# Kernel optimization log

Measured on AMD Instinct MI355X. Metric: run time of the kernel, lower is better.

## Reference

```python
import jax, jax.numpy as jnp
import numpy as np

N = 50000
E = 800000
F_IN = 512
HID = 32
HEADS = 8
CLS = 64
NEG_SLOPE = 0.2
EPS = 1e-16  # PyG softmax denominator epsilon


def setup_inputs() -> dict:
    key = jax.random.key(0)
    ks = jax.random.split(key, 10)
    x = jax.random.normal(ks[0], (N, F_IN), dtype=jnp.float32)
    edge_index = jax.random.randint(ks[1], (2, E), 0, N, dtype=jnp.int64)
    # layer 1: in=F_IN, heads=HEADS, out_per_head=HID, concat
    s1 = 1.0 / np.sqrt(F_IN)
    W1 = jax.random.normal(ks[2], (F_IN, HEADS * HID), dtype=jnp.float32) * s1
    att_src1 = jax.random.normal(ks[3], (HEADS, HID), dtype=jnp.float32) * 0.1
    att_dst1 = jax.random.normal(ks[4], (HEADS, HID), dtype=jnp.float32) * 0.1
    b1 = jnp.zeros((HEADS * HID,), dtype=jnp.float32)
    # layer 2: in=HEADS*HID, heads=1, out=CLS, no concat
    s2 = 1.0 / np.sqrt(HEADS * HID)
    W2 = jax.random.normal(ks[5], (HEADS * HID, CLS), dtype=jnp.float32) * s2
    att_src2 = jax.random.normal(ks[6], (1, CLS), dtype=jnp.float32) * 0.1
    att_dst2 = jax.random.normal(ks[7], (1, CLS), dtype=jnp.float32) * 0.1
    b2 = jnp.zeros((CLS,), dtype=jnp.float32)
    return {"x": x, "edge_index": edge_index,
            "W1": W1, "att_src1": att_src1, "att_dst1": att_dst1, "b1": b1,
            "W2": W2, "att_src2": att_src2, "att_dst2": att_dst2, "b2": b2}


def gat_conv(x, edge_index, W, att_src, att_dst, bias, concat):
    n = x.shape[0]
    heads, c = att_src.shape
    h = (x @ W).reshape(n, heads, c)                       # [N,H,C]
    # add self loops (PyG GATConv default)
    loop = jnp.arange(n, dtype=edge_index.dtype)
    src = jnp.concatenate([edge_index[0], loop])
    dst = jnp.concatenate([edge_index[1], loop])
    a_src = jnp.einsum('nhc,hc->nh', h, att_src)           # [N,H]
    a_dst = jnp.einsum('nhc,hc->nh', h, att_dst)
    e = a_src[src] + a_dst[dst]                            # [E',H]
    e = jax.nn.leaky_relu(e, NEG_SLOPE)
    # segment softmax over destination node
    m = jax.ops.segment_max(e, dst, num_segments=n)
    e = jnp.exp(e - jax.lax.stop_gradient(m)[dst])
    s = jax.ops.segment_sum(e, dst, num_segments=n)
    alpha = e / (s[dst] + EPS)                             # [E',H]
    msg = h[src] * alpha[:, :, None]                       # [E',H,C]
    out = jax.ops.segment_sum(msg, dst, num_segments=n)    # [N,H,C]
    out = out.reshape(n, heads * c) if concat else out.mean(axis=1)
    return out + bias


def reference(x, edge_index, W1, att_src1, att_dst1, b1, W2, att_src2, att_dst2, b2):
    h = gat_conv(x, edge_index, W1, att_src1, att_dst1, b1, concat=True)
    h = jax.nn.relu(h)
    # F.dropout with training=False (eval) is identity
    h = gat_conv(h, edge_index, W2, att_src2, att_dst2, b2, concat=False)
    return jax.nn.log_softmax(h, axis=1)
```

## Files before the change

kernel.cpp:

```cpp
#include <hip/hip_runtime.h>
#include <hip/hip_bf16.h>
#include <stdint.h>

#define F_IN 512
#define HID 32
#define HEADS 8
#define C1 (HEADS*HID)
#define CLS 64
#define NEG 0.2f
#define EPS 1e-16f

typedef __bf16 bf16x8 __attribute__((ext_vector_type(8)));
typedef __bf16 bf16x4 __attribute__((ext_vector_type(4)));
typedef float  f32x4  __attribute__((ext_vector_type(4)));

__device__ __forceinline__ float leaky(float v) { return v > 0.f ? v : NEG * v; }

__device__ __forceinline__ bf16x8 cvt8(float4 a, float4 b) {
  bf16x8 o;
  o[0] = (__bf16)a.x; o[1] = (__bf16)a.y; o[2] = (__bf16)a.z; o[3] = (__bf16)a.w;
  o[4] = (__bf16)b.x; o[5] = (__bf16)b.y; o[6] = (__bf16)b.z; o[7] = (__bf16)b.w;
  return o;
}

__global__ __launch_bounds__(256) void prep(const float* __restrict__ W1,
    const float* __restrict__ W2, const int* __restrict__ ei,
    __bf16* __restrict__ w1t, __bf16* __restrict__ w2t,
    int* __restrict__ deg, int E) {
  const int b = blockIdx.x, t = threadIdx.x;
  if (b < 64) {
    int i = b * 256 + t;
    int o0 = i * 8;
    int c = o0 >> 9, k0 = o0 & 511;
    bf16x8 o;
#pragma unroll
    for (int j = 0; j < 8; j++) o[j] = (__bf16)W1[(size_t)(k0 + j) * C1 + c];
    *(bf16x8*)(w1t + (size_t)o0) = o;
  } else if (b < 72) {
    int i = (b - 64) * 256 + t;
    int o0 = i * 8;
    int c = o0 >> 8, k0 = o0 & 255;
    bf16x8 o;
#pragma unroll
    for (int j = 0; j < 8; j++) o[j] = (__bf16)W2[(size_t)(k0 + j) * CLS + c];
    *(bf16x8*)(w2t + (size_t)o0) = o;
  } else {
    int e = (b - 72) * 256 + t;
    if (e < E) atomicAdd(&deg[ei[E + e]], 1);
  }
}

__global__ __launch_bounds__(256) void scan_k1(const int* __restrict__ deg,
    int* __restrict__ bsum, int N) {
  __shared__ int ws[4];
  const int t = threadIdx.x, lane = t & 63, wid = t >> 6;
  int i = blockIdx.x * 256 + t;
  int v = (i < N) ? deg[i] : 0;
#pragma unroll
  for (int o = 1; o < 64; o <<= 1) v += __shfl_xor(v, o);
  if (lane == 0) ws[wid] = v;
  __syncthreads();
  if (t == 0) bsum[blockIdx.x] = ws[0] + ws[1] + ws[2] + ws[3];
}

__global__ __launch_bounds__(256) void scan_k2(int* __restrict__ bsum, int nb) {
  __shared__ int wsum[4];
  __shared__ int carry_s;
  const int t = threadIdx.x, lane = t & 63, wid = t >> 6;
  if (t == 0) carry_s = 0;
  __syncthreads();
  for (int base = 0; base < nb; base += 256) {
    int i = base + t;
    int v = (i < nb) ? bsum[i] : 0;
    int inc = v;
#pragma unroll
    for (int o = 1; o < 64; o <<= 1) { int x = __shfl_up(inc, o); if (lane >= o) inc += x; }
    if (lane == 63) wsum[wid] = inc;
    __syncthreads();
    int woff = 0;
    for (int w = 0; w < wid; w++) woff += wsum[w];
    int excl = carry_s + woff + inc - v;
    if (i < nb) bsum[i] = excl;
    __syncthreads();
    if (t == 0) carry_s += wsum[0] + wsum[1] + wsum[2] + wsum[3];
    __syncthreads();
  }
}

__global__ __launch_bounds__(256) void scan_k3(const int* __restrict__ deg,
    const int* __restrict__ bsum, int* __restrict__ rowstart,
    int* __restrict__ cur, int N) {
  __shared__ int wsum[4];
  const int t = threadIdx.x, lane = t & 63, wid = t >> 6;
  int i = blockIdx.x * 256 + t;
  int v = (i < N) ? deg[i] : 0;
  int inc = v;
#pragma unroll
  for (int o = 1; o < 64; o <<= 1) { int x = __shfl_up(inc, o); if (lane >= o) inc += x; }
  if (lane == 63) wsum[wid] = inc;
  __syncthreads();
  int woff = 0;
  for (int w = 0; w < wid; w++) woff += wsum[w];
  int excl = bsum[blockIdx.x] + woff + inc - v;
  if (i < N) { rowstart[i] = excl; cur[i] = excl; }
  if (i == N - 1) rowstart[N] = excl + v;
}

__global__ __launch_bounds__(256) void scatter_csr(const int* __restrict__ ei,
    int* __restrict__ cur, int* __restrict__ csr_src, int E) {
  int e = blockIdx.x * 256 + threadIdx.x;
  if (e >= E) return;
  int s = ei[e], d = ei[E + e];
  int pos = atomicAdd(&cur[d], 1);
  csr_src[pos] = s;
}

__global__ __launch_bounds__(256) void gemm1_fused(const float* __restrict__ A,
    const __bf16* __restrict__ Bt, __bf16* __restrict__ C,
    const float* __restrict__ asw, const float* __restrict__ adw,
    float* __restrict__ a_src, float* __restrict__ a_dst, int M) {
  __shared__ __bf16 Al[128 * 32];
  __shared__ __bf16 Bl[128 * 32];
  const int tid = threadIdx.x, lane = tid & 63, wave = tid >> 6;
  const int lm = lane & 15, q = lane >> 4;
  const int wr = (wave >> 1) * 64, wc = (wave & 1) * 64;
  const int bm = blockIdx.y * 128, bn = blockIdx.x * 128;
  const int srow = tid >> 2, skc = (tid & 3) * 8;

  f32x4 acc[4][4];
#pragma unroll
  for (int i = 0; i < 4; i++)
#pragma unroll
    for (int j = 0; j < 4; j++) acc[i][j] = (f32x4){0.f, 0.f, 0.f, 0.f};

  const int ra0 = min(bm + srow, M - 1);
  const int ra1 = min(bm + srow + 64, M - 1);
  const int rb0 = bn + srow, rb1 = bn + srow + 64;

  float4 a00, a01, a10, a11;
  bf16x8 vb0, vb1;
  a00 = *(const float4*)(A + (size_t)ra0 * 512 + skc);
  a01 = *(const float4*)(A + (size_t)ra0 * 512 + skc + 4);
  a10 = *(const float4*)(A + (size_t)ra1 * 512 + skc);
  a11 = *(const float4*)(A + (size_t)ra1 * 512 + skc + 4);
  vb0 = *(const bf16x8*)(Bt + (size_t)rb0 * 512 + skc);
  vb1 = *(const bf16x8*)(Bt + (size_t)rb1 * 512 + skc);

  for (int kk = 0; kk < 16; kk++) {
    __syncthreads();
    *(bf16x8*)(Al + srow * 32 + skc)        = cvt8(a00, a01);
    *(bf16x8*)(Al + (srow + 64) * 32 + skc) = cvt8(a10, a11);
    *(bf16x8*)(Bl + srow * 32 + skc)        = vb0;
    *(bf16x8*)(Bl + (srow + 64) * 32 + skc) = vb1;
    __syncthreads();
    if (kk + 1 < 16) {
      const int k0 = (kk + 1) * 32;
      a00 = *(const float4*)(A + (size_t)ra0 * 512 + k0 + skc);
      a01 = *(const float4*)(A + (size_t)ra0 * 512 + k0 + skc + 4);
      a10 = *(const float4*)(A + (size_t)ra1 * 512 + k0 + skc);
      a11 = *(const float4*)(A + (size_t)ra1 * 512 + k0 + skc + 4);
      vb0 = *(const bf16x8*)(Bt + (size_t)rb0 * 512 + k0 + skc);
      vb1 = *(const bf16x8*)(Bt + (size_t)rb1 * 512 + k0 + skc);
    }
    bf16x8 af[4], bfr[4];
#pragma unroll
    for (int mi = 0; mi < 4; mi++)
      af[mi] = *(const bf16x8*)(Al + (wr + mi * 16 + lm) * 32 + q * 8);
#pragma unroll
    for (int ni = 0; ni < 4; ni++)
      bfr[ni] = *(const bf16x8*)(Bl + (wc + ni * 16 + lm) * 32 + q * 8);
#pragma unroll
    for (int mi = 0; mi < 4; mi++)
#pragma unroll
      for (int ni = 0; ni < 4; ni++)
        acc[mi][ni] = __builtin_amdgcn_mfma_f32_16x16x32_bf16(af[mi], bfr[ni], acc[mi][ni], 0, 0, 0);
  }

#pragma unroll
  for (int mi = 0; mi < 4; mi++) {
#pragma unroll
    for (int ni = 0; ni < 4; ni++) {
      const int col = bn + wc + ni * 16 + lm;
#pragma unroll
      for (int r = 0; r < 4; r++) {
        const int row = bm + wr + mi * 16 + q * 4 + r;
        if (row < M) C[(size_t)row * C1 + col] = (__bf16)acc[mi][ni][r];
      }
    }
  }

  {
    const int cb = bn + wc;
    const int h0 = cb >> 5;
    float ws[4], wd[4];
#pragma unroll
    for (int ni = 0; ni < 4; ni++) {
      ws[ni] = asw[cb + ni * 16 + lm];
      wd[ni] = adw[cb + ni * 16 + lm];
    }
#pragma unroll
    for (int mi = 0; mi < 4; mi++) {
#pragma unroll
      for (int r = 0; r < 4; r++) {
        float ps0 = acc[mi][0][r] * ws[0] + acc[mi][1][r] * ws[1];
        float ps1 = acc[mi][2][r] * ws[2] + acc[mi][3][r] * ws[3];
        float pd0 = acc[mi][0][r] * wd[0] + acc[mi][1][r] * wd[1];
        float pd1 = acc[mi][2][r] * wd[2] + acc[mi][3][r] * wd[3];
#pragma unroll
        for (int o = 1; o <= 8; o <<= 1) {
          ps0 += __shfl_xor(ps0, o); ps1 += __shfl_xor(ps1, o);
          pd0 += __shfl_xor(pd0, o); pd1 += __shfl_xor(pd1, o);
        }
        if (lm == 0) {
          const int row = bm + wr + mi * 16 + q * 4 + r;
          if (row < M) {
            a_src[(size_t)row * 8 + h0]     = ps0;
            a_src[(size_t)row * 8 + h0 + 1] = ps1;
            a_dst[(size_t)row * 8 + h0]     = pd0;
            a_dst[(size_t)row * 8 + h0 + 1] = pd1;
          }
        }
      }
    }
  }
}

__global__ __launch_bounds__(256) void gemm2_fused(const __bf16* __restrict__ A,
    const __bf16* __restrict__ Bt, __bf16* __restrict__ C,
    const float* __restrict__ asw, const float* __restrict__ adw,
    float* __restrict__ a_src, float* __restrict__ a_dst, int M) {
  __shared__ __bf16 Al[128 * 32];
  __shared__ __bf16 Bl[64 * 32];
  __shared__ float sred[128][2][2];
  const int tid = threadIdx.x, lane = tid & 63, wave = tid >> 6;
  const int lm = lane & 15, q = lane >> 4;
  const int wr = (wave >> 1) * 64, wc = (wave & 1) * 32;
  const int bm = blockIdx.x * 128;
  const int srow = tid >> 2, skc = (tid & 3) * 8;

  f32x4 acc[4][2];
#pragma unroll
  for (int i = 0; i < 4; i++)
#pragma unroll
    for (int j = 0; j < 2; j++) acc[i][j] = (f32x4){0.f, 0.f, 0.f, 0.f};

  const int ra0 = min(bm + srow, M - 1);
  const int ra1 = min(bm + srow + 64, M - 1);

  bf16x8 va0, va1, vb;
  va0 = *(const bf16x8*)(A + (size_t)ra0 * C1 + skc);
  va1 = *(const bf16x8*)(A + (size_t)ra1 * C1 + skc);
  vb  = *(const bf16x8*)(Bt + (size_t)srow * C1 + skc);

  for (int kk = 0; kk < 8; kk++) {
    __syncthreads();
    *(bf16x8*)(Al + srow * 32 + skc)        = va0;
    *(bf16x8*)(Al + (srow + 64) * 32 + skc) = va1;
    *(bf16x8*)(Bl + srow * 32 + skc)        = vb;
    __syncthreads();
    if (kk + 1 < 8) {
      const int k0 = (kk + 1) * 32;
      va0 = *(const bf16x8*)(A + (size_t)ra0 * C1 + k0 + skc);
      va1 = *(const bf16x8*)(A + (size_t)ra1 * C1 + k0 + skc);
      vb  = *(const bf16x8*)(Bt + (size_t)srow * C1 + k0 + skc);
    }
    bf16x8 af[4], bfr[2];
#pragma unroll
    for (int mi = 0; mi < 4; mi++)
      af[mi] = *(const bf16x8*)(Al + (wr + mi * 16 + lm) * 32 + q * 8);
#pragma unroll
    for (int ni = 0; ni < 2; ni++)
      bfr[ni] = *(const bf16x8*)(Bl + (wc + ni * 16 + lm) * 32 + q * 8);
#pragma unroll
    for (int mi = 0; mi < 4; mi++)
#pragma unroll
      for (int ni = 0; ni < 2; ni++)
        acc[mi][ni] = __builtin_amdgcn_mfma_f32_16x16x32_bf16(af[mi], bfr[ni], acc[mi][ni], 0, 0, 0);
  }

  float ws[2], wd[2];
#pragma unroll
  for (int ni = 0; ni < 2; ni++) {
    ws[ni] = asw[wc + ni * 16 + lm];
    wd[ni] = adw[wc + ni * 16 + lm];
  }
#pragma unroll
  for (int mi = 0; mi < 4; mi++) {
#pragma unroll
    for (int ni = 0; ni < 2; ni++) {
      const int col = wc + ni * 16 + lm;
#pragma unroll
      for (int r = 0; r < 4; r++) {
        const int row = bm + wr + mi * 16 + q * 4 + r;
        if (row < M) C[(size_t)row * CLS + col] = (__bf16)acc[mi][ni][r];
      }
    }
#pragma unroll
    for (int r = 0; r < 4; r++) {
      float ps = acc[mi][0][r] * ws[0] + acc[mi][1][r] * ws[1];
      float pd = acc[mi][0][r] * wd[0] + acc[mi][1][r] * wd[1];
#pragma unroll
      for (int o = 1; o <= 8; o <<= 1) { ps += __shfl_xor(ps, o); pd += __shfl_xor(pd, o); }
      if (lm == 0) {
        const int rl = wr + mi * 16 + q * 4 + r;
        sred[rl][wave & 1][0] = ps;
        sred[rl][wave & 1][1] = pd;
      }
    }
  }
  __syncthreads();
  if (tid < 128) {
    const int row = bm + tid;
    if (row < M) {
      a_src[row] = sred[tid][0][0] + sred[tid][1][0];
      a_dst[row] = sred[tid][0][1] + sred[tid][1][1];
    }
  }
}

__global__ __launch_bounds__(256) void gather1(const int* __restrict__ rowstart,
    const int* __restrict__ csr_src, const __bf16* __restrict__ h1,
    const float* __restrict__ as1, const float* __restrict__ ad1,
    const float* __restrict__ b1, __bf16* __restrict__ o1, int N) {
  const int t = threadIdx.x;
  const int d = blockIdx.x * 4 + (t >> 6);
  if (d >= N) return;
  const int lane = t & 63;
  const int e8 = lane >> 3, hh = lane & 7;
  const int r0 = rowstart[d];
  const int deg = rowstart[d + 1] - r0;

  const float addh = ad1[(size_t)d * 8 + hh];
  const float self_sc = leaky(as1[(size_t)d * 8 + hh] + addh);

  int   se[8];
  float sc[8];
#pragma unroll
  for (int ch = 0; ch < 8; ch++) {
    const int j = ch * 8 + e8;
    se[ch] = 0; sc[ch] = -3.4e38f;
    if (j < deg) {
      int s = csr_src[r0 + j];
      se[ch] = s;
      sc[ch] = leaky(as1[(size_t)s * 8 + hh] + addh);
    }
  }
  float mx = -3.4e38f;
#pragma unroll
  for (int ch = 0; ch < 8; ch++) mx = fmaxf(mx, sc[ch]);
  for (int j0 = 64; j0 < deg; j0 += 8) {
    int j = j0 + e8;
    if (j < deg) {
      int s = csr_src[r0 + j];
      mx = fmaxf(mx, leaky(as1[(size_t)s * 8 + hh] + addh));
    }
  }
  mx = fmaxf(mx, __shfl_xor(mx, 8));
  mx = fmaxf(mx, __shfl_xor(mx, 16));
  mx = fmaxf(mx, __shfl_xor(mx, 32));
  mx = fmaxf(mx, self_sc);

  float sum = 0.f;
#pragma unroll
  for (int ch = 0; ch < 8; ch++)
    if (ch * 8 + e8 < deg) sum += __expf(sc[ch] - mx);
  for (int j0 = 64; j0 < deg; j0 += 8) {
    int j = j0 + e8;
    if (j < deg) {
      int s = csr_src[r0 + j];
      sum += __expf(leaky(as1[(size_t)s * 8 + hh] + addh) - mx);
    }
  }
  sum += __shfl_xor(sum, 8);
  sum += __shfl_xor(sum, 16);
  sum += __shfl_xor(sum, 32);
  sum += __expf(self_sc - mx);
  const float inv = 1.f / (sum + EPS);

  float al[8];
#pragma unroll
  for (int ch = 0; ch < 8; ch++) al[ch] = __expf(sc[ch] - mx) * inv;
  const float al_self_byhh = __expf(self_sc - mx) * inv;

  const int p = lane >> 5, g = lane & 31, hg = g >> 2;
  float acc[8];
#pragma unroll
  for (int i = 0; i < 8; i++) acc[i] = 0.f;

#pragma unroll
  for (int it = 0; it < 32; it++) {
    if (it * 2 < deg) {
      const int   j   = it * 2 + p;
      const int   s_j = __shfl(se[it >> 2], (j & 7) * 8);
      const float a_j = __shfl(al[it >> 2], (j & 7) * 8 + hg);
      bf16x8 x = *(const bf16x8*)(h1 + (size_t)s_j * C1 + g * 8);
#pragma unroll
      for (int i = 0; i < 8; i++) acc[i] += a_j * (float)x[i];
    }
  }
  for (int j0 = 64; j0 < deg; j0 += 8) {
    int j = j0 + e8;
    int se2 = 0; float al2 = 0.f;
    if (j < deg) { se2 = csr_src[r0 + j]; al2 = __expf(leaky(as1[(size_t)se2 * 8 + hh] + addh) - mx) * inv; }
#pragma unroll
    for (int it = 0; it < 4; it++) {
      if (j0 + it * 2 < deg) {
        const int   jj  = it * 2 + p;
        const int   s_j = __shfl(se2, jj * 8);
        const float a_j = __shfl(al2, jj * 8 + hg);
        bf16x8 x = *(const bf16x8*)(h1 + (size_t)s_j * C1 + g * 8);
#pragma unroll
        for (int i = 0; i < 8; i++) acc[i] += a_j * (float)x[i];
      }
    }
  }
#pragma unroll
  for (int i = 0; i < 8; i++) acc[i] += __shfl_xor(acc[i], 32);

  const float a_selfh = __shfl(al_self_byhh, hg);
  if (lane < 32) {
    bf16x8 xs = *(const bf16x8*)(h1 + (size_t)d * C1 + g * 8);
    const float4 b4a = *(const float4*)(b1 + g * 8);
    const float4 b4b = *(const float4*)(b1 + g * 8 + 4);
    bf16x8 o;
    o[0] = (__bf16)fmaxf(acc[0] + a_selfh * (float)xs[0] + b4a.x, 0.f);
    o[1] = (__bf16)fmaxf(acc[1] + a_selfh * (float)xs[1] + b4a.y, 0.f);
    o[2] = (__bf16)fmaxf(acc[2] + a_selfh * (float)xs[2] + b4a.z, 0.f);
    o[3] = (__bf16)fmaxf(acc[3] + a_selfh * (float)xs[3] + b4a.w, 0.f);
    o[4] = (__bf16)fmaxf(acc[4] + a_selfh * (float)xs[4] + b4b.x, 0.f);
    o[5] = (__bf16)fmaxf(acc[5] + a_selfh * (float)xs[5] + b4b.y, 0.f);
    o[6] = (__bf16)fmaxf(acc[6] + a_selfh * (float)xs[6] + b4b.z, 0.f);
    o[7] = (__bf16)fmaxf(acc[7] + a_selfh * (float)xs[7] + b4b.w, 0.f);
    *(bf16x8*)(o1 + (size_t)d * C1 + g * 8) = o;
  }
}

__global__ __launch_bounds__(256) void gather2(const int* __restrict__ rowstart,
    const int* __restrict__ csr_src, const __bf16* __restrict__ h2b,
    const float* __restrict__ as2, const float* __restrict__ ad2,
    const float* __restrict__ b2, float* __restrict__ out, int N) {
  const int t = threadIdx.x, lane = t & 63;
  const int d = blockIdx.x * 4 + (t >> 6);
  if (d >= N) return;
  const int r0 = rowstart[d], deg = rowstart[d + 1] - r0;
  const float addd = ad2[d];
  const float self_e = __expf(leaky(as2[d] + addd));

  int se = 0; float ex = 0.f;
  if (lane < deg) { se = csr_src[r0 + lane]; ex = __expf(leaky(as2[se] + addd)); }
  float sum = ex;
  for (int j0 = 64; j0 < deg; j0 += 64) {
    int j = j0 + lane;
    if (j < deg) sum += __expf(leaky(as2[csr_src[r0 + j]] + addd));
  }
#pragma unroll
  for (int o = 1; o < 64; o <<= 1) sum += __shfl_xor(sum, o);
  sum += self_e;
  const float inv = 1.f / (sum + EPS);
  const float alpha = ex * inv;
  const float al_self = self_e * inv;

  const int e8 = lane >> 3, c8 = lane & 7;
  float acc[8];
#pragma unroll
  for (int i = 0; i < 8; i++) acc[i] = 0.f;

#pragma unroll
  for (int itg = 0; itg < 8; itg += 2) {
    if (itg * 8 < deg) {
      const int   sa = __shfl(se, itg * 8 + e8);
      const int   sb = __shfl(se, itg * 8 + 8 + e8);
      const float aa = __shfl(alpha, itg * 8 + e8);
      const float ab = __shfl(alpha, itg * 8 + 8 + e8);
      bf16x8 xa = *(const bf16x8*)(h2b + ((uint32_t)sa * 64u + (uint32_t)(c8 * 8)));
      bf16x8 xb = *(const bf16x8*)(h2b + ((uint32_t)sb * 64u + (uint32_t)(c8 * 8)));
#pragma unroll
      for (int i = 0; i < 8; i++) acc[i] += aa * (float)xa[i];
#pragma unroll
      for (int i = 0; i < 8; i++) acc[i] += ab * (float)xb[i];
    }
  }
  for (int j0 = 64; j0 < deg; j0 += 64) {
    int j = j0 + lane;
    int se2 = 0; float al2 = 0.f;
    if (j < deg) { se2 = csr_src[r0 + j]; al2 = __expf(leaky(as2[se2] + addd)) * inv; }
#pragma unroll
    for (int it = 0; it < 8; it++) {
      if (j0 + it * 8 < deg) {
        const int   jj  = it * 8 + e8;
        const int   s_j = __shfl(se2, jj);
        const float a_j = __shfl(al2, jj);
        bf16x8 x = *(const bf16x8*)(h2b + ((uint32_t)s_j * 64u + (uint32_t)(c8 * 8)));
#pragma unroll
        for (int i = 0; i < 8; i++) acc[i] += a_j * (float)x[i];
      }
    }
  }
#pragma unroll
  for (int i = 0; i < 8; i++) {
    acc[i] += __shfl_xor(acc[i], 8);
    acc[i] += __shfl_xor(acc[i], 16);
    acc[i] += __shfl_xor(acc[i], 32);
  }

  bf16x8 xs = *(const bf16x8*)(h2b + ((uint32_t)d * 64u + (uint32_t)(c8 * 8)));
  const float4 bba = *(const float4*)(b2 + c8 * 8);
  const float4 bbb = *(const float4*)(b2 + c8 * 8 + 4);
  float v[8];
  v[0] = acc[0] + al_self * (float)xs[0] + bba.x;
  v[1] = acc[1] + al_self * (float)xs[1] + bba.y;
  v[2] = acc[2] + al_self * (float)xs[2] + bba.z;
  v[3] = acc[3] + al_self * (float)xs[3] + bba.w;
  v[4] = acc[4] + al_self * (float)xs[4] + bbb.x;
  v[5] = acc[5] + al_self * (float)xs[5] + bbb.y;
  v[6] = acc[6] + al_self * (float)xs[6] + bbb.z;
  v[7] = acc[7] + al_self * (float)xs[7] + bbb.w;
  float m2 = v[0];
#pragma unroll
  for (int i = 1; i < 8; i++) m2 = fmaxf(m2, v[i]);
  m2 = fmaxf(m2, __shfl_xor(m2, 1));
  m2 = fmaxf(m2, __shfl_xor(m2, 2));
  m2 = fmaxf(m2, __shfl_xor(m2, 4));
  float sm = 0.f;
#pragma unroll
  for (int i = 0; i < 8; i++) sm += __expf(v[i] - m2);
  sm += __shfl_xor(sm, 1);
  sm += __shfl_xor(sm, 2);
  sm += __shfl_xor(sm, 4);
  const float lg = m2 + __logf(sm);
  if (lane < 8) {
    float4 o0, o1v;
    o0.x  = v[0] - lg; o0.y  = v[1] - lg; o0.z  = v[2] - lg; o0.w  = v[3] - lg;
    o1v.x = v[4] - lg; o1v.y = v[5] - lg; o1v.z = v[6] - lg; o1v.w = v[7] - lg;
    *(float4*)(out + (size_t)d * CLS + c8 * 8)     = o0;
    *(float4*)(out + (size_t)d * CLS + c8 * 8 + 4) = o1v;
  }
}

extern "C" void kernel_launch(void* const* d_in, const int* in_sizes, int n_in,
                              void* d_out, int out_size, void* d_ws, size_t ws_size,
                              hipStream_t stream) {
  const float* x        = (const float*)d_in[0];
  const int*   ei       = (const int*)d_in[1];
  const float* W1       = (const float*)d_in[2];
  const float* att_src1 = (const float*)d_in[3];
  const float* att_dst1 = (const float*)d_in[4];
  const float* b1       = (const float*)d_in[5];
  const float* W2       = (const float*)d_in[6];
  const float* att_src2 = (const float*)d_in[7];
  const float* att_dst2 = (const float*)d_in[8];
  const float* b2       = (const float*)d_in[9];
  float* out = (float*)d_out;

  const int N  = in_sizes[0] / F_IN;
  const int E  = in_sizes[1] / 2;
  const int NB = (N + 255) / 256;

  char* ws = (char*)d_ws;
  size_t off = 0;
  auto alloc = [&](size_t bytes) -> void* {
    void* p = ws + off;
    off += (bytes + 255) & ~(size_t)255;
    return p;
  };
  __bf16* h1  = (__bf16*)alloc((size_t)N * C1 * 2);
  __bf16* o1  = (__bf16*)alloc((size_t)N * C1 * 2);
  float*  as1 = (float*)alloc((size_t)N * HEADS * 4);
  float*  ad1 = (float*)alloc((size_t)N * HEADS * 4);
  __bf16* h2b = (__bf16*)alloc((size_t)N * CLS * 2);
  float*  as2 = (float*)alloc((size_t)N * 4);
  float*  ad2 = (float*)alloc((size_t)N * 4);
  int* deg      = (int*)alloc((size_t)N * 4);
  int* rowstart = (int*)alloc((size_t)(N + 1) * 4);
  int* cur      = (int*)alloc((size_t)N * 4);
  int* csr_src  = (int*)alloc((size_t)E * 4);
  int* bsum     = (int*)alloc((size_t)NB * 4);
  __bf16* w1t = (__bf16*)alloc((size_t)C1 * F_IN * 2);
  __bf16* w2t = (__bf16*)alloc((size_t)CLS * C1 * 2);

  hipMemsetAsync(deg, 0, (size_t)N * 4, stream);
  prep<<<72 + (E + 255) / 256, 256, 0, stream>>>(W1, W2, ei, w1t, w2t, deg, E);

  scan_k1<<<NB, 256, 0, stream>>>(deg, bsum, N);
  scan_k2<<<1, 256, 0, stream>>>(bsum, NB);
  scan_k3<<<NB, 256, 0, stream>>>(deg, bsum, rowstart, cur, N);
  scatter_csr<<<(E + 255) / 256, 256, 0, stream>>>(ei, cur, csr_src, E);

  {
    dim3 g(C1 / 128, (N + 127) / 128);
    gemm1_fused<<<g, 256, 0, stream>>>(x, w1t, h1, att_src1, att_dst1, as1, ad1, N);
  }
  gather1<<<(N + 3) / 4, 256, 0, stream>>>(rowstart, csr_src, h1, as1, ad1, b1, o1, N);

  gemm2_fused<<<(N + 127) / 128, 256, 0, stream>>>(o1, w2t, h2b, att_src2, att_dst2, as2, ad2, N);
  gather2<<<(N + 3) / 4, 256, 0, stream>>>(rowstart, csr_src, h2b, as2, ad2, b2, out, N);
}
```

Before: 405.9 us.

## Cover all 256 output columns per GEMM1 block to read x once

GEMM1 now launches one 512-thread block per 128-row tile and covers all 256 output columns, instead of two 256-thread blocks that split the columns. Each row of the fp32 input x is therefore loaded and converted to bf16 once rather than twice, removing duplicate global traffic on the largest input. In exchange the block needs twice the LDS for B, has fewer blocks in the grid, and puts eight waves behind each barrier.

```diff
diff --git a/kernel.cpp b/kernel.cpp
--- a/kernel.cpp
+++ b/kernel.cpp
@@ -115,16 +115,17 @@
   csr_src[pos] = s;
 }
 
-__global__ __launch_bounds__(256) void gemm1_fused(const float* __restrict__ A,
+__global__ __launch_bounds__(512) void gemm1_fused(const float* __restrict__ A,
     const __bf16* __restrict__ Bt, __bf16* __restrict__ C,
     const float* __restrict__ asw, const float* __restrict__ adw,
     float* __restrict__ a_src, float* __restrict__ a_dst, int M) {
   __shared__ __bf16 Al[128 * 32];
-  __shared__ __bf16 Bl[128 * 32];
+  __shared__ __bf16 Bl[256 * 32];
   const int tid = threadIdx.x, lane = tid & 63, wave = tid >> 6;
   const int lm = lane & 15, q = lane >> 4;
-  const int wr = (wave >> 1) * 64, wc = (wave & 1) * 64;
-  const int bm = blockIdx.y * 128, bn = blockIdx.x * 128;
+  const int wr = ((wave >> 1) & 1) * 64;
+  const int cb = (wave >> 2) * 128 + (wave & 1) * 64;
+  const int bm = blockIdx.x * 128;
   const int srow = tid >> 2, skc = (tid & 3) * 8;
 
   f32x4 acc[4][4];
@@ -133,34 +134,27 @@
 #pragma unroll
     for (int j = 0; j < 4; j++) acc[i][j] = (f32x4){0.f, 0.f, 0.f, 0.f};
 
-  const int ra0 = min(bm + srow, M - 1);
-  const int ra1 = min(bm + srow + 64, M - 1);
-  const int rb0 = bn + srow, rb1 = bn + srow + 64;
-
-  float4 a00, a01, a10, a11;
+  const int ra = min(bm + srow, M - 1);
+
+  float4 a0, a1;
   bf16x8 vb0, vb1;
-  a00 = *(const float4*)(A + (size_t)ra0 * 512 + skc);
-  a01 = *(const float4*)(A + (size_t)ra0 * 512 + skc + 4);
-  a10 = *(const float4*)(A + (size_t)ra1 * 512 + skc);
-  a11 = *(const float4*)(A + (size_t)ra1 * 512 + skc + 4);
-  vb0 = *(const bf16x8*)(Bt + (size_t)rb0 * 512 + skc);
-  vb1 = *(const bf16x8*)(Bt + (size_t)rb1 * 512 + skc);
+  a0  = *(const float4*)(A + (size_t)ra * 512 + skc);
+  a1  = *(const float4*)(A + (size_t)ra * 512 + skc + 4);
+  vb0 = *(const bf16x8*)(Bt + (size_t)srow * 512 + skc);
+  vb1 = *(const bf16x8*)(Bt + (size_t)(srow + 128) * 512 + skc);
 
   for (int kk = 0; kk < 16; kk++) {
     __syncthreads();
-    *(bf16x8*)(Al + srow * 32 + skc)        = cvt8(a00, a01);
-    *(bf16x8*)(Al + (srow + 64) * 32 + skc) = cvt8(a10, a11);
-    *(bf16x8*)(Bl + srow * 32 + skc)        = vb0;
-    *(bf16x8*)(Bl + (srow + 64) * 32 + skc) = vb1;
+    *(bf16x8*)(Al + srow * 32 + skc)         = cvt8(a0, a1);
+    *(bf16x8*)(Bl + srow * 32 + skc)         = vb0;
+    *(bf16x8*)(Bl + (srow + 128) * 32 + skc) = vb1;
     __syncthreads();
     if (kk + 1 < 16) {
       const int k0 = (kk + 1) * 32;
-      a00 = *(const float4*)(A + (size_t)ra0 * 512 + k0 + skc);
-      a01 = *(const float4*)(A + (size_t)ra0 * 512 + k0 + skc + 4);
-      a10 = *(const float4*)(A + (size_t)ra1 * 512 + k0 + skc);
-      a11 = *(const float4*)(A + (size_t)ra1 * 512 + k0 + skc + 4);
-      vb0 = *(const bf16x8*)(Bt + (size_t)rb0 * 512 + k0 + skc);
-      vb1 = *(const bf16x8*)(Bt + (size_t)rb1 * 512 + k0 + skc);
+      a0  = *(const float4*)(A + (size_t)ra * 512 + k0 + skc);
+      a1  = *(const float4*)(A + (size_t)ra * 512 + k0 + skc + 4);
+      vb0 = *(const bf16x8*)(Bt + (size_t)srow * 512 + k0 + skc);
+      vb1 = *(const bf16x8*)(Bt + (size_t)(srow + 128) * 512 + k0 + skc);
     }
     bf16x8 af[4], bfr[4];
 #pragma unroll
@@ -168,7 +162,7 @@
       af[mi] = *(const bf16x8*)(Al + (wr + mi * 16 + lm) * 32 + q * 8);
 #pragma unroll
     for (int ni = 0; ni < 4; ni++)
-      bfr[ni] = *(const bf16x8*)(Bl + (wc + ni * 16 + lm) * 32 + q * 8);
+      bfr[ni] = *(const bf16x8*)(Bl + (cb + ni * 16 + lm) * 32 + q * 8);
 #pragma unroll
     for (int mi = 0; mi < 4; mi++)
 #pragma unroll
@@ -180,7 +174,7 @@
   for (int mi = 0; mi < 4; mi++) {
 #pragma unroll
     for (int ni = 0; ni < 4; ni++) {
-      const int col = bn + wc + ni * 16 + lm;
+      const int col = cb + ni * 16 + lm;
 #pragma unroll
       for (int r = 0; r < 4; r++) {
         const int row = bm + wr + mi * 16 + q * 4 + r;
@@ -190,7 +184,6 @@
   }
 
   {
-    const int cb = bn + wc;
     const int h0 = cb >> 5;
     float ws[4], wd[4];
 #pragma unroll
@@ -586,10 +579,7 @@
   scan_k3<<<NB, 256, 0, stream>>>(deg, bsum, rowstart, cur, N);
   scatter_csr<<<(E + 255) / 256, 256, 0, stream>>>(ei, cur, csr_src, E);
 
-  {
-    dim3 g(C1 / 128, (N + 127) / 128);
-    gemm1_fused<<<g, 256, 0, stream>>>(x, w1t, h1, att_src1, att_dst1, as1, ad1, N);
-  }
+  gemm1_fused<<<(N + 127) / 128, 512, 0, stream>>>(x, w1t, h1, att_src1, att_dst1, as1, ad1, N);
   gather1<<<(N + 3) / 4, 256, 0, stream>>>(rowstart, csr_src, h1, as1, ad1, b1, o1, N);
 
   gemm2_fused<<<(N + 127) / 128, 256, 0, stream>>>(o1, w2t, h2b, att_src2, att_dst2, as2, ad2, N);
```

After: 393.8 us (median of 2 runs). -3.0%, faster.
